# Optimization experiments

Hardware: AMD Instinct MI355X
Metric: run time of the kernel (lower is better)

Reference implementation:

```python
import jax, jax.numpy as jnp
import numpy as np

B = 4096
INPUT_DIM = 1024
ARG_IN = 8
IN_HIDDEN = 64
OUT_HIDDEN = [4096, 4096, 4096]
NUM_CELL_TYPES = 16
NUM_CLASSES = 10
LN_EPS = 1e-5


def _xavier(key, shape):
    # shape = (..., fan_in, fan_out); xavier uniform like torch init
    fan_in, fan_out = shape[-2], shape[-1]
    lim = float(np.sqrt(6.0 / (fan_in + fan_out)))
    return jax.random.uniform(key, shape, jnp.float32, -lim, lim)


def setup_inputs() -> dict:
    key = jax.random.key(0)
    ks = jax.random.split(key, 12)
    prev = OUT_HIDDEN[0] // ARG_IN  # 512
    inp = {
        "x": jax.random.normal(ks[0], (B, INPUT_DIM), jnp.float32),
        "labels": jax.random.randint(ks[1], (B,), 0, NUM_CLASSES),
        # outer nets (stored as (in, out))
        "Wout0": _xavier(ks[2], (INPUT_DIM, OUT_HIDDEN[0])),
        "bout0": jnp.zeros((OUT_HIDDEN[0],), jnp.float32),
        "Wout1": _xavier(ks[3], (prev, OUT_HIDDEN[1])),
        "bout1": jnp.zeros((OUT_HIDDEN[1],), jnp.float32),
        "Wout2": _xavier(ks[4], (prev, OUT_HIDDEN[2])),
        "bout2": jnp.zeros((OUT_HIDDEN[2],), jnp.float32),
        # per-cell-type inner MLPs, stacked over group dim T
        "W1": _xavier(ks[5], (NUM_CELL_TYPES, ARG_IN, IN_HIDDEN)),
        "b1": jnp.zeros((NUM_CELL_TYPES, IN_HIDDEN), jnp.float32),
        "W2": _xavier(ks[6], (NUM_CELL_TYPES, IN_HIDDEN, IN_HIDDEN)),
        "b2": jnp.zeros((NUM_CELL_TYPES, IN_HIDDEN), jnp.float32),
        "W3": _xavier(ks[7], (NUM_CELL_TYPES, IN_HIDDEN, 1))[..., 0],  # (T, H)
        "b3": jnp.zeros((NUM_CELL_TYPES,), jnp.float32),
        # output head
        "Wfc": _xavier(ks[8], (prev, NUM_CLASSES)),
        "bfc": jnp.zeros((NUM_CLASSES,), jnp.float32),
    }
    return inp


def _layernorm(x):
    mu = jnp.mean(x, axis=-1, keepdims=True)
    var = jnp.var(x, axis=-1, keepdims=True)
    return (x - mu) * jax.lax.rsqrt(var + LN_EPS)


def _inner_mlps(out, W1, b1, W2, b2, W3, b3):
    # out: (B, D) with D = T * Cg * ARG_IN; grouped tiny MLPs, vectorized over T
    bsz = out.shape[0]
    z = out.reshape(bsz, NUM_CELL_TYPES, -1, ARG_IN)  # (B, T, Cg, A)
    h = jax.nn.relu(jnp.einsum("btca,tah->btch", z, W1) + b1[None, :, None, :])
    h = jax.nn.relu(jnp.einsum("btch,thk->btck", h, W2) + b2[None, :, None, :])
    y = jnp.einsum("btch,th->btc", h, W3) + b3[None, :, None]  # (B, T, Cg)
    return y.reshape(bsz, -1)  # (B, T*Cg)


def reference(x, labels, Wout0, bout0, Wout1, bout1, Wout2, bout2,
              W1, b1, W2, b2, W3, b3, Wfc, bfc):
    outs = [(Wout0, bout0), (Wout1, bout1), (Wout2, bout2)]
    out = x.reshape(x.shape[0], -1)
    for W, b in outs:
        out = _layernorm(out @ W + b)
        out = _inner_mlps(out, W1, b1, W2, b2, W3, b3)
        # dropout p=0.0 -> identity
    logits = out @ Wfc + bfc  # (B, num_classes)
    logp = jax.nn.log_softmax(logits, axis=-1)
    loss = -jnp.mean(jnp.take_along_axis(logp, labels[:, None], axis=1))
    return logits, loss
```

## Files before the change

kernel.cpp:

```cpp
#include <hip/hip_runtime.h>
#include <hip/hip_bf16.h>
#include <math.h>

constexpr int BATCH   = 4096;
constexpr int NCLS    = 10;
constexpr int NHID    = 4096;
constexpr int PREV    = 512;
constexpr int NTYPES  = 16;
constexpr int CG      = 32;
constexpr float LN_EPS = 1e-5f;

typedef __attribute__((ext_vector_type(8))) short short8;
typedef __attribute__((ext_vector_type(4))) float f32x4;

__global__ __launch_bounds__(256)
void gemm_mfma_kernel(const __hip_bfloat16* __restrict__ A,
                      const __hip_bfloat16* __restrict__ BT,
                      const float* __restrict__ bias,
                      float* __restrict__ C,
                      int N, int K) {
  __shared__ __hip_bfloat16 As[128 * 32];
  __shared__ __hip_bfloat16 Bs[128 * 32];
  const int tid  = threadIdx.x;
  const int wid  = tid >> 6;
  const int lane = tid & 63;
  const int row0 = blockIdx.y * 128;
  const int col0 = blockIdx.x * 128;
  const int wrow = (wid >> 1) * 64;
  const int wcol = (wid & 1) * 64;

  f32x4 acc[4][4] = {};

  const int sr = wid * 32;
  const int lr = lane >> 2;
  const int lc = (lane & 3) * 8;

  const int fr = lane & 15;
  const int fo = (lane >> 4) * 8;

  for (int k0 = 0; k0 < K; k0 += 32) {
    const __hip_bfloat16* ga0 = A  + (size_t)(row0 + sr +      lr) * K + k0 + lc;
    const __hip_bfloat16* ga1 = A  + (size_t)(row0 + sr + 16 + lr) * K + k0 + lc;
    const __hip_bfloat16* gb0 = BT + (size_t)(col0 + sr +      lr) * K + k0 + lc;
    const __hip_bfloat16* gb1 = BT + (size_t)(col0 + sr + 16 + lr) * K + k0 + lc;
    __builtin_amdgcn_global_load_lds((const __attribute__((address_space(1))) void*)ga0,
                                     (__attribute__((address_space(3))) void*)&As[(sr     ) * 32], 16, 0, 0);
    __builtin_amdgcn_global_load_lds((const __attribute__((address_space(1))) void*)ga1,
                                     (__attribute__((address_space(3))) void*)&As[(sr + 16) * 32], 16, 0, 0);
    __builtin_amdgcn_global_load_lds((const __attribute__((address_space(1))) void*)gb0,
                                     (__attribute__((address_space(3))) void*)&Bs[(sr     ) * 32], 16, 0, 0);
    __builtin_amdgcn_global_load_lds((const __attribute__((address_space(1))) void*)gb1,
                                     (__attribute__((address_space(3))) void*)&Bs[(sr + 16) * 32], 16, 0, 0);
    __syncthreads();

    short8 af[4], bfr[4];
    #pragma unroll
    for (int i = 0; i < 4; ++i)
      af[i] = *reinterpret_cast<const short8*>(&As[(wrow + i * 16 + fr) * 32 + fo]);
    #pragma unroll
    for (int j = 0; j < 4; ++j)
      bfr[j] = *reinterpret_cast<const short8*>(&Bs[(wcol + j * 16 + fr) * 32 + fo]);

    #pragma unroll
    for (int i = 0; i < 4; ++i)
      #pragma unroll
      for (int j = 0; j < 4; ++j)
        acc[i][j] = __builtin_amdgcn_mfma_f32_16x16x32_bf16(af[i], bfr[j], acc[i][j], 0, 0, 0);
    __syncthreads();
  }

  #pragma unroll
  for (int j = 0; j < 4; ++j) {
    const int cc = col0 + wcol + j * 16 + (lane & 15);
    const float bv = bias[cc];
    #pragma unroll
    for (int i = 0; i < 4; ++i) {
      const int rr = row0 + wrow + i * 16 + (lane >> 4) * 4;
      #pragma unroll
      for (int r = 0; r < 4; ++r)
        C[(size_t)(rr + r) * N + cc] = acc[i][j][r] + bv;
    }
  }
}

__global__ __launch_bounds__(256)
void cvt_bf16_kernel(const float* __restrict__ in, __hip_bfloat16* __restrict__ out, int n) {
  const int i = (blockIdx.x * 256 + threadIdx.x) * 4;
  if (i >= n) return;
  const float4 v = *reinterpret_cast<const float4*>(&in[i]);
  __hip_bfloat16 t[4];
  t[0] = __float2bfloat16(v.x); t[1] = __float2bfloat16(v.y);
  t[2] = __float2bfloat16(v.z); t[3] = __float2bfloat16(v.w);
  *reinterpret_cast<ushort4*>(&out[i]) = *reinterpret_cast<const ushort4*>(t);
}

__global__ __launch_bounds__(256)
void transpose_cvt_kernel(const float* __restrict__ W, __hip_bfloat16* __restrict__ WT,
                          int K, int N) {
  __shared__ __hip_bfloat16 tile[64][65];
  const int tid = threadIdx.x;
  const int kt = blockIdx.y * 64, nt = blockIdx.x * 64;
  const int cn = tid & 63;
  for (int r = tid >> 6; r < 64; r += 4)
    tile[cn][r] = __float2bfloat16(W[(size_t)(kt + r) * N + nt + cn]);
  __syncthreads();
  for (int r = tid >> 6; r < 64; r += 4)
    WT[(size_t)(nt + r) * K + kt + cn] = tile[r][cn];
}

__global__ __launch_bounds__(256)
void prep_weights_kernel(const float* __restrict__ W2, const float* __restrict__ W1,
                         __hip_bfloat16* __restrict__ W2Tb,
                         __hip_bfloat16* __restrict__ W1b,
                         float* __restrict__ swsum) {
  const int t = blockIdx.x;
  for (int idx = threadIdx.x; idx < 64 * 64; idx += 256) {
    const int n = idx >> 6, h = idx & 63;
    W2Tb[t * 4096 + n * 64 + h] = __float2bfloat16(W2[t * 4096 + h * 64 + n]);
  }
  for (int idx = threadIdx.x; idx < 512; idx += 256) {
    const int n = idx >> 3, k = idx & 7;
    W1b[t * 512 + idx] = __float2bfloat16(W1[t * 512 + k * 64 + n]);
  }
  if (threadIdx.x < 64) {
    float s = 0.f;
    #pragma unroll
    for (int k = 0; k < 8; ++k) s += W1[t * 512 + k * 64 + threadIdx.x];
    swsum[t * 64 + threadIdx.x] = s;
  }
}

__global__ __launch_bounds__(256)
void ln_stats_kernel(const float* __restrict__ X, float2* __restrict__ stats) {
  const int lane = threadIdx.x & 63;
  const int row  = blockIdx.x * 4 + (threadIdx.x >> 6);
  const float* p = X + (size_t)row * NHID;
  float s = 0.f, ss = 0.f;
  #pragma unroll
  for (int i = 0; i < 16; ++i) {
    const float4 v = *reinterpret_cast<const float4*>(&p[i * 256 + lane * 4]);
    s  += v.x + v.y + v.z + v.w;
    ss += v.x * v.x + v.y * v.y + v.z * v.z + v.w * v.w;
  }
  #pragma unroll
  for (int off = 32; off; off >>= 1) { s += __shfl_xor(s, off); ss += __shfl_xor(ss, off); }
  if (lane == 0) {
    const float mu = s * (1.f / 4096.f);
    float2 st;
    st.x = mu;
    st.y = rsqrtf(ss * (1.f / 4096.f) - mu * mu + LN_EPS);
    stats[row] = st;
  }
}

__global__ __launch_bounds__(256, 2)
void inner_type_kernel(const float* __restrict__ X,
                       const float2* __restrict__ stats,
                       float* __restrict__ out,
                       __hip_bfloat16* __restrict__ outb,
                       const __hip_bfloat16* __restrict__ W2Tb,
                       const __hip_bfloat16* __restrict__ W1b,
                       const float* __restrict__ swsum,
                       const float* __restrict__ b1,
                       const float* __restrict__ b2,
                       const float* __restrict__ W3, const float* __restrict__ b3) {
  __shared__ __hip_bfloat16 H1s[128 * 64];
  const int tid  = threadIdx.x;
  const int lane = tid & 63;
  const int wvid = tid >> 6;
  const int t    = blockIdx.y;
  const int r0   = blockIdx.x * 64;

  const int fc  = lane & 15;
  const int fq  = lane >> 4;
  const bool ld = (fq == 0);

  const float* zcol = X + t * 256 + fc * 8;

#define LOAD_Z(zr, itv)                                                        \
  if (ld) {                                                                    \
    const float* zb_ = zcol + (size_t)(r0 + (itv) * 4 + wvid) * NHID;          \
    *reinterpret_cast<float4*>(&zr[0])  = *reinterpret_cast<const float4*>(zb_);          \
    *reinterpret_cast<float4*>(&zr[4])  = *reinterpret_cast<const float4*>(zb_ + 4);      \
    *reinterpret_cast<float4*>(&zr[8])  = *reinterpret_cast<const float4*>(zb_ + 128);    \
    *reinterpret_cast<float4*>(&zr[12]) = *reinterpret_cast<const float4*>(zb_ + 132);    \
  }

  float zA[16], zB[16];
  #pragma unroll
  for (int i = 0; i < 16; ++i) { zA[i] = 0.f; zB[i] = 0.f; }
  float2 stA, stB;
  LOAD_Z(zA, 0);
  stA = stats[r0 + wvid];

  short8 w1frag[4];
  #pragma unroll
  for (int nf = 0; nf < 4; ++nf) {
    short8 v = {};
    if (ld) v = *reinterpret_cast<const short8*>(&W1b[(size_t)t * 512 + (nf * 16 + fc) * 8]);
    w1frag[nf] = v;
  }

  short8 bfrag[4][2];
  #pragma unroll
  for (int cf = 0; cf < 4; ++cf)
    #pragma unroll
    for (int ks = 0; ks < 2; ++ks)
      bfrag[cf][ks] = *reinterpret_cast<const short8*>(
          &W2Tb[(size_t)t * 4096 + (cf * 16 + fc) * 64 + ks * 32 + fq * 8]);

  float4 b1q[4], swq[4];
  #pragma unroll
  for (int nf = 0; nf < 4; ++nf) {
    b1q[nf] = *reinterpret_cast<const float4*>(&b1[t * 64 + nf * 16 + fq * 4]);
    swq[nf] = *reinterpret_cast<const float4*>(&swsum[t * 64 + nf * 16 + fq * 4]);
  }

  float b2v[4], w3v[4];
  #pragma unroll
  for (int cf = 0; cf < 4; ++cf) {
    b2v[cf] = b2[t * 64 + cf * 16 + fc];
    w3v[cf] = W3[t * 64 + cf * 16 + fc];
  }
  const float yb = b3[t];

#define BODY(zr, stv, itv)                                                     \
  {                                                                            \
    const int row_ = r0 + (itv) * 4 + wvid;                                    \
    const float rs_ = stv.y;                                                   \
    const float c1_ = -stv.x * rs_;                                            \
            \
    short8 zf[2];                                                              \
    {                                                                          \
      union { short8 v; __hip_bfloat16 e[8]; } p0, p1;                         \
      _Pragma("unroll")                                                        \
      for (int q = 0; q < 8; ++q) {                                            \
        p0.e[q] = __float2bfloat16(zr[q]);                                     \
        p1.e[q] = __float2bfloat16(zr[8 + q]);                                 \
      }                                                                        \
      zf[0] = p0.v; zf[1] = p1.v;                                              \
    }                                                                          \
                  \
    f32x4 pC[4][2] = {};                                                       \
    _Pragma("unroll")                                                          \
    for (int nf = 0; nf < 4; ++nf) {                                           \
      pC[nf][0] = __builtin_amdgcn_mfma_f32_16x16x32_bf16(w1frag[nf], zf[0], pC[nf][0], 0, 0, 0); \
      pC[nf][1] = __builtin_amdgcn_mfma_f32_16x16x32_bf16(w1frag[nf], zf[1], pC[nf][1], 0, 0, 0); \
    }                                                                          \
        \
    _Pragma("unroll")                                                          \
    for (int nf = 0; nf < 4; ++nf) {                                           \
      const float bx = fmaf(c1_, swq[nf].x, b1q[nf].x);                        \
      const float by = fmaf(c1_, swq[nf].y, b1q[nf].y);                        \
      const float bz = fmaf(c1_, swq[nf].z, b1q[nf].z);                        \
      const float bw = fmaf(c1_, swq[nf].w, b1q[nf].w);                        \
      _Pragma("unroll")                                                        \
      for (int ci = 0; ci < 2; ++ci) {                                         \
        union { uint2 u; __hip_bfloat16 e[4]; } pk_;                           \
        pk_.e[0] = __float2bfloat16(fmaxf(fmaf(rs_, pC[nf][ci][0], bx), 0.f)); \
        pk_.e[1] = __float2bfloat16(fmaxf(fmaf(rs_, pC[nf][ci][1], by), 0.f)); \
        pk_.e[2] = __float2bfloat16(fmaxf(fmaf(rs_, pC[nf][ci][2], bz), 0.f)); \
        pk_.e[3] = __float2bfloat16(fmaxf(fmaf(rs_, pC[nf][ci][3], bw), 0.f)); \
        const int cell_ = wvid * 32 + ci * 16 + fc;                            \
        const int boff_ = cell_ * 128 + ((nf * 32 + fq * 8) ^ ((cell_ & 7) << 4)); \
        *reinterpret_cast<uint2*>((char*)H1s + boff_) = pk_.u;                 \
      }                                                                        \
    }                                                                          \
                  \
    f32x4 acc[2][4] = {};                                                      \
    _Pragma("unroll")                                                          \
    for (int ks = 0; ks < 2; ++ks) {                                           \
      short8 a0_, a1_;                                                         \
      {                                                                        \
        const int hrow_ = wvid * 32 + fc;                                      \
        a0_ = *reinterpret_cast<const short8*>(                                \
            &H1s[hrow_ * 64 + ((ks * 32 + fq * 8) ^ ((hrow_ & 7) << 3))]);     \
      }                                                                        \
      {                                                                        \
        const int hrow_ = wvid * 32 + 16 + fc;                                 \
        a1_ = *reinterpret_cast<const short8*>(                                \
            &H1s[hrow_ * 64 + ((ks * 32 + fq * 8) ^ ((hrow_ & 7) << 3))]);     \
      }                                                                        \
      _Pragma("unroll")                                                        \
      for (int cf = 0; cf < 4; ++cf) {                                         \
        acc[0][cf] = __builtin_amdgcn_mfma_f32_16x16x32_bf16(a0_, bfrag[cf][ks], acc[0][cf], 0, 0, 0); \
        acc[1][cf] = __builtin_amdgcn_mfma_f32_16x16x32_bf16(a1_, bfrag[cf][ks], acc[1][cf], 0, 0, 0); \
      }                                                                        \
    }                                                                          \
                                                              \
    float p[2][4];                                                             \
    _Pragma("unroll")                                                          \
    for (int rf = 0; rf < 2; ++rf)                                             \
      _Pragma("unroll")                                                        \
      for (int r = 0; r < 4; ++r) {                                            \
        float s_ = 0.f;                                                        \
        _Pragma("unroll")                                                      \
        for (int cf = 0; cf < 4; ++cf)                                         \
          s_ = fmaf(fmaxf(acc[rf][cf][r] + b2v[cf], 0.f), w3v[cf], s_);        \
        s_ += __shfl_xor(s_, 1);                                               \
        s_ += __shfl_xor(s_, 2);                                               \
        s_ += __shfl_xor(s_, 4);                                               \
        s_ += __shfl_xor(s_, 8);                                               \
        p[rf][r] = s_;                                                         \
      }                                                                        \
    if (fc == 0) {                                                             \
      _Pragma("unroll")                                                        \
      for (int rf = 0; rf < 2; ++rf)                                           \
        _Pragma("unroll")                                                      \
        for (int r = 0; r < 4; ++r) {                                          \
          const int c_ = rf * 16 + fq * 4 + r;                                 \
          const float y_ = p[rf][r] + yb;                                      \
          const size_t oidx_ = (size_t)row_ * PREV + t * CG + c_;              \
          if (out) out[oidx_] = y_;                                            \
          outb[oidx_] = __float2bfloat16(y_);                                  \
        }                                                                      \
    }                                                                          \
  }

  #pragma unroll 1
  for (int it2 = 0; it2 < 8; ++it2) {
    const int itA = it2 * 2;
    LOAD_Z(zB, itA + 1);
    stB = stats[r0 + (itA + 1) * 4 + wvid];
    BODY(zA, stA, itA);
    if (it2 < 7) {
      LOAD_Z(zA, itA + 2);
      stA = stats[r0 + (itA + 2) * 4 + wvid];
    }
    BODY(zB, stB, itA + 1);
  }
#undef LOAD_Z
#undef BODY
}

__global__ __launch_bounds__(64)
void head_kernel(const float* __restrict__ Y, const float* __restrict__ Wfc,
                 const float* __restrict__ bfc, const int* __restrict__ labels,
                 float* __restrict__ logits, float* __restrict__ rowloss) {
  const int b = blockIdx.x;
  const int lane = threadIdx.x;
  const float* yr = Y + (size_t)b * PREV;
  float acc[NCLS] = {};
  for (int k = lane; k < PREV; k += 64) {
    const float yv = yr[k];
    #pragma unroll
    for (int cI = 0; cI < NCLS; ++cI) acc[cI] = fmaf(yv, Wfc[k * NCLS + cI], acc[cI]);
  }
  #pragma unroll
  for (int cI = 0; cI < NCLS; ++cI) {
    #pragma unroll
    for (int off = 32; off; off >>= 1) acc[cI] += __shfl_down(acc[cI], off);
  }
  if (lane == 0) {
    float l[NCLS];
    float m = -1e30f;
    #pragma unroll
    for (int cI = 0; cI < NCLS; ++cI) { l[cI] = acc[cI] + bfc[cI]; m = fmaxf(m, l[cI]); }
    float se = 0.f;
    #pragma unroll
    for (int cI = 0; cI < NCLS; ++cI) se += __expf(l[cI] - m);
    const float lse = m + __logf(se);
    #pragma unroll
    for (int cI = 0; cI < NCLS; ++cI) logits[(size_t)b * NCLS + cI] = l[cI];
    const int lab = labels[b];
    float picked = 0.f;
    #pragma unroll
    for (int cI = 0; cI < NCLS; ++cI) picked += (cI == lab) ? l[cI] : 0.f;
    rowloss[b] = lse - picked;
  }
}

__global__ __launch_bounds__(256)
void loss_reduce_kernel(const float* __restrict__ rowloss, float* __restrict__ loss_out) {
  float s = 0.f;
  for (int i = threadIdx.x; i < BATCH; i += 256) s += rowloss[i];
  #pragma unroll
  for (int off = 32; off; off >>= 1) s += __shfl_down(s, off);
  __shared__ float sb[4];
  if ((threadIdx.x & 63) == 0) sb[threadIdx.x >> 6] = s;
  __syncthreads();
  if (threadIdx.x == 0) loss_out[0] = (sb[0] + sb[1] + sb[2] + sb[3]) * (1.f / BATCH);
}

extern "C" void kernel_launch(void* const* d_in, const int* in_sizes, int n_in,
                              void* d_out, int out_size, void* d_ws, size_t ws_size,
                              hipStream_t stream) {
  const float* x      = (const float*)d_in[0];
  const int*   labels = (const int*)  d_in[1];
  const float* Wout0  = (const float*)d_in[2];
  const float* bout0  = (const float*)d_in[3];
  const float* Wout1  = (const float*)d_in[4];
  const float* bout1  = (const float*)d_in[5];
  const float* Wout2  = (const float*)d_in[6];
  const float* bout2  = (const float*)d_in[7];
  const float* W1     = (const float*)d_in[8];
  const float* b1     = (const float*)d_in[9];
  const float* W2     = (const float*)d_in[10];
  const float* b2     = (const float*)d_in[11];
  const float* W3     = (const float*)d_in[12];
  const float* b3     = (const float*)d_in[13];
  const float* Wfc    = (const float*)d_in[14];
  const float* bfc    = (const float*)d_in[15];

  char* ws = (char*)d_ws;
  float*          Abuf    = (float*)(ws);
  float*          Ybuf    = (float*)(ws + ((size_t)64 << 20));
  __hip_bfloat16* Ybf     = (__hip_bfloat16*)(ws + ((size_t)72 << 20));
  __hip_bfloat16* xbf     = (__hip_bfloat16*)(ws + ((size_t)76 << 20));
  __hip_bfloat16* WT0     = (__hip_bfloat16*)(ws + ((size_t)84 << 20));
  __hip_bfloat16* WT1     = (__hip_bfloat16*)(ws + ((size_t)92 << 20));
  __hip_bfloat16* WT2     = (__hip_bfloat16*)(ws + ((size_t)96 << 20));
  __hip_bfloat16* W2Tb    = (__hip_bfloat16*)(ws + ((size_t)100 << 20));
  __hip_bfloat16* W1b     = (__hip_bfloat16*)(ws + ((size_t)100 << 20) + (128 << 10));
  float*          swsum   = (float*)(ws + ((size_t)100 << 20) + (192 << 10));
  float*          rowloss = (float*)(ws + ((size_t)101 << 20));
  float2*         stats   = (float2*)(ws + ((size_t)101 << 20) + (256 << 10));

  float* logits = (float*)d_out;
  float* loss   = logits + (size_t)BATCH * NCLS;

  cvt_bf16_kernel<<<dim3(BATCH * 1024 / 4 / 256), dim3(256), 0, stream>>>(x, xbf, BATCH * 1024);
  transpose_cvt_kernel<<<dim3(NHID / 64, 1024 / 64), dim3(256), 0, stream>>>(Wout0, WT0, 1024, NHID);
  transpose_cvt_kernel<<<dim3(NHID / 64, PREV / 64), dim3(256), 0, stream>>>(Wout1, WT1, PREV, NHID);
  transpose_cvt_kernel<<<dim3(NHID / 64, PREV / 64), dim3(256), 0, stream>>>(Wout2, WT2, PREV, NHID);
  prep_weights_kernel<<<dim3(NTYPES), dim3(256), 0, stream>>>(W2, W1, W2Tb, W1b, swsum);

  const dim3 ggrid(NHID / 128, BATCH / 128), gblk(256);
  const dim3 sgrid(BATCH / 4), sblk(256);
  const dim3 igrid(BATCH / 64, NTYPES), iblk(256);

  gemm_mfma_kernel<<<ggrid, gblk, 0, stream>>>(xbf, WT0, bout0, Abuf, NHID, 1024);
  ln_stats_kernel<<<sgrid, sblk, 0, stream>>>(Abuf, stats);
  inner_type_kernel<<<igrid, iblk, 0, stream>>>(Abuf, stats, nullptr, Ybf, W2Tb, W1b, swsum, b1, b2, W3, b3);
  gemm_mfma_kernel<<<ggrid, gblk, 0, stream>>>(Ybf, WT1, bout1, Abuf, NHID, PREV);
  ln_stats_kernel<<<sgrid, sblk, 0, stream>>>(Abuf, stats);
  inner_type_kernel<<<igrid, iblk, 0, stream>>>(Abuf, stats, nullptr, Ybf, W2Tb, W1b, swsum, b1, b2, W3, b3);
  gemm_mfma_kernel<<<ggrid, gblk, 0, stream>>>(Ybf, WT2, bout2, Abuf, NHID, PREV);
  ln_stats_kernel<<<sgrid, sblk, 0, stream>>>(Abuf, stats);
  inner_type_kernel<<<igrid, iblk, 0, stream>>>(Abuf, stats, Ybuf, Ybf, W2Tb, W1b, swsum, b1, b2, W3, b3);

  head_kernel<<<dim3(BATCH), dim3(64), 0, stream>>>(Ybuf, Wfc, bfc, labels, logits, rowloss);
  loss_reduce_kernel<<<dim3(1), dim3(256), 0, stream>>>(rowloss, loss);
}
```

Baseline: 380.4 us.

## Fuse LayerNorm statistics into GEMM epilogue and store activations as bf16

The GEMM epilogue now writes its output as bf16 instead of fp32 and computes per-row partial sums and sums of squares for each column block. A small reduce kernel turns those partials into mean and rstd, replacing the full-row stats pass that reread the fp32 matrix. The inner MLP kernel reads bf16 directly, which removes its in-register conversion, and it is relaunched with half the rows per block at higher occupancy. The intent is to cut HBM traffic for the large intermediate. The trade-off is that pre-LN values are rounded to bf16, and the variance uses single-pass sum and sum-of-squares accumulation.

```diff
diff --git a/kernel.cpp b/kernel.cpp
--- a/kernel.cpp
+++ b/kernel.cpp
@@ -8,19 +8,22 @@
 constexpr int PREV    = 512;
 constexpr int NTYPES  = 16;
 constexpr int CG      = 32;
+constexpr int NCB     = NHID / 128;
 constexpr float LN_EPS = 1e-5f;
 
 typedef __attribute__((ext_vector_type(8))) short short8;
 typedef __attribute__((ext_vector_type(4))) float f32x4;
 
 __global__ __launch_bounds__(256)
-void gemm_mfma_kernel(const __hip_bfloat16* __restrict__ A,
-                      const __hip_bfloat16* __restrict__ BT,
-                      const float* __restrict__ bias,
-                      float* __restrict__ C,
-                      int N, int K) {
+void gemm_ln_kernel(const __hip_bfloat16* __restrict__ A,
+                    const __hip_bfloat16* __restrict__ BT,
+                    const float* __restrict__ bias,
+                    __hip_bfloat16* __restrict__ Cb,
+                    float2* __restrict__ partials,
+                    int K) {
   __shared__ __hip_bfloat16 As[128 * 32];
   __shared__ __hip_bfloat16 Bs[128 * 32];
+  __shared__ float2 sbuf[2][128];
   const int tid  = threadIdx.x;
   const int wid  = tid >> 6;
   const int lane = tid & 63;
@@ -36,7 +39,8 @@
   const int lc = (lane & 3) * 8;
 
   const int fr = lane & 15;
-  const int fo = (lane >> 4) * 8;
+  const int lq = lane >> 4;
+  const int fo = lq * 8;
 
   for (int k0 = 0; k0 < K; k0 += 32) {
     const __hip_bfloat16* ga0 = A  + (size_t)(row0 + sr +      lr) * K + k0 + lc;
@@ -69,18 +73,53 @@
     __syncthreads();
   }
 
+  float sA[4][4] = {}, sQ[4][4] = {};
   #pragma unroll
   for (int j = 0; j < 4; ++j) {
-    const int cc = col0 + wcol + j * 16 + (lane & 15);
+    const int cc = col0 + wcol + j * 16 + fr;
     const float bv = bias[cc];
     #pragma unroll
     for (int i = 0; i < 4; ++i) {
-      const int rr = row0 + wrow + i * 16 + (lane >> 4) * 4;
+      const int rr = row0 + wrow + i * 16 + lq * 4;
       #pragma unroll
-      for (int r = 0; r < 4; ++r)
-        C[(size_t)(rr + r) * N + cc] = acc[i][j][r] + bv;
+      for (int r = 0; r < 4; ++r) {
+        const float v = acc[i][j][r] + bv;
+        Cb[(size_t)(rr + r) * NHID + cc] = __float2bfloat16(v);
+        sA[i][r] += v;
+        sQ[i][r] = fmaf(v, v, sQ[i][r]);
+      }
     }
   }
+  #pragma unroll
+  for (int i = 0; i < 4; ++i)
+    #pragma unroll
+    for (int r = 0; r < 4; ++r) {
+      float sv = sA[i][r], sq = sQ[i][r];
+      sv += __shfl_xor(sv, 1); sq += __shfl_xor(sq, 1);
+      sv += __shfl_xor(sv, 2); sq += __shfl_xor(sq, 2);
+      sv += __shfl_xor(sv, 4); sq += __shfl_xor(sq, 4);
+      sv += __shfl_xor(sv, 8); sq += __shfl_xor(sq, 8);
+      if (fr == 0) sbuf[wid & 1][wrow + i * 16 + lq * 4 + r] = make_float2(sv, sq);
+    }
+  __syncthreads();
+  for (int idx = tid; idx < 128; idx += 256) {
+    const float2 a = sbuf[0][idx], b = sbuf[1][idx];
+    partials[(size_t)(row0 + idx) * NCB + blockIdx.x] = make_float2(a.x + b.x, a.y + b.y);
+  }
+}
+
+__global__ __launch_bounds__(256)
+void stats_reduce_kernel(const float2* __restrict__ partials, float2* __restrict__ stats) {
+  const int row = blockIdx.x * 256 + threadIdx.x;
+  const float2* p = partials + (size_t)row * NCB;
+  float s = 0.f, ss = 0.f;
+  #pragma unroll
+  for (int cb = 0; cb < NCB; ++cb) { const float2 v = p[cb]; s += v.x; ss += v.y; }
+  const float mu = s * (1.f / 4096.f);
+  float2 st;
+  st.x = mu;
+  st.y = rsqrtf(ss * (1.f / 4096.f) - mu * mu + LN_EPS);
+  stats[row] = st;
 }
 
 __global__ __launch_bounds__(256)
@@ -130,31 +169,8 @@
   }
 }
 
-__global__ __launch_bounds__(256)
-void ln_stats_kernel(const float* __restrict__ X, float2* __restrict__ stats) {
-  const int lane = threadIdx.x & 63;
-  const int row  = blockIdx.x * 4 + (threadIdx.x >> 6);
-  const float* p = X + (size_t)row * NHID;
-  float s = 0.f, ss = 0.f;
-  #pragma unroll
-  for (int i = 0; i < 16; ++i) {
-    const float4 v = *reinterpret_cast<const float4*>(&p[i * 256 + lane * 4]);
-    s  += v.x + v.y + v.z + v.w;
-    ss += v.x * v.x + v.y * v.y + v.z * v.z + v.w * v.w;
-  }
-  #pragma unroll
-  for (int off = 32; off; off >>= 1) { s += __shfl_xor(s, off); ss += __shfl_xor(ss, off); }
-  if (lane == 0) {
-    const float mu = s * (1.f / 4096.f);
-    float2 st;
-    st.x = mu;
-    st.y = rsqrtf(ss * (1.f / 4096.f) - mu * mu + LN_EPS);
-    stats[row] = st;
-  }
-}
-
-__global__ __launch_bounds__(256, 2)
-void inner_type_kernel(const float* __restrict__ X,
+__global__ __launch_bounds__(256, 3)
+void inner_type_kernel(const __hip_bfloat16* __restrict__ Xb,
                        const float2* __restrict__ stats,
                        float* __restrict__ out,
                        __hip_bfloat16* __restrict__ outb,
@@ -169,28 +185,24 @@
   const int lane = tid & 63;
   const int wvid = tid >> 6;
   const int t    = blockIdx.y;
-  const int r0   = blockIdx.x * 64;
+  const int r0   = blockIdx.x * 32;
 
   const int fc  = lane & 15;
   const int fq  = lane >> 4;
   const bool ld = (fq == 0);
 
-  const float* zcol = X + t * 256 + fc * 8;
-
-#define LOAD_Z(zr, itv)                                                        \
+  const __hip_bfloat16* zcol = Xb + t * 256 + fc * 8;
+
+#define LOAD_Z(zf0, zf1, itv)                                                  \
   if (ld) {                                                                    \
-    const float* zb_ = zcol + (size_t)(r0 + (itv) * 4 + wvid) * NHID;          \
-    *reinterpret_cast<float4*>(&zr[0])  = *reinterpret_cast<const float4*>(zb_);          \
-    *reinterpret_cast<float4*>(&zr[4])  = *reinterpret_cast<const float4*>(zb_ + 4);      \
-    *reinterpret_cast<float4*>(&zr[8])  = *reinterpret_cast<const float4*>(zb_ + 128);    \
-    *reinterpret_cast<float4*>(&zr[12]) = *reinterpret_cast<const float4*>(zb_ + 132);    \
-  }
-
-  float zA[16], zB[16];
-  #pragma unroll
-  for (int i = 0; i < 16; ++i) { zA[i] = 0.f; zB[i] = 0.f; }
+    const __hip_bfloat16* zb_ = zcol + (size_t)(r0 + (itv) * 4 + wvid) * NHID; \
+    zf0 = *reinterpret_cast<const short8*>(zb_);                               \
+    zf1 = *reinterpret_cast<const short8*>(zb_ + 128);                         \
+  }
+
+  short8 zfA0 = {}, zfA1 = {}, zfB0 = {}, zfB1 = {};
   float2 stA, stB;
-  LOAD_Z(zA, 0);
+  LOAD_Z(zfA0, zfA1, 0);
   stA = stats[r0 + wvid];
 
   short8 w1frag[4];
@@ -224,30 +236,19 @@
   }
   const float yb = b3[t];
 
-#define BODY(zr, stv, itv)                                                     \
+#define BODY(zf0, zf1, stv, itv)                                               \
   {                                                                            \
     const int row_ = r0 + (itv) * 4 + wvid;                                    \
     const float rs_ = stv.y;                                                   \
     const float c1_ = -stv.x * rs_;                                            \
-            \
-    short8 zf[2];                                                              \
-    {                                                                          \
-      union { short8 v; __hip_bfloat16 e[8]; } p0, p1;                         \
-      _Pragma("unroll")                                                        \
-      for (int q = 0; q < 8; ++q) {                                            \
-        p0.e[q] = __float2bfloat16(zr[q]);                                     \
-        p1.e[q] = __float2bfloat16(zr[8 + q]);                                 \
-      }                                                                        \
-      zf[0] = p0.v; zf[1] = p1.v;                                              \
-    }                                                                          \
-                  \
+                   \
     f32x4 pC[4][2] = {};                                                       \
     _Pragma("unroll")                                                          \
     for (int nf = 0; nf < 4; ++nf) {                                           \
-      pC[nf][0] = __builtin_amdgcn_mfma_f32_16x16x32_bf16(w1frag[nf], zf[0], pC[nf][0], 0, 0, 0); \
-      pC[nf][1] = __builtin_amdgcn_mfma_f32_16x16x32_bf16(w1frag[nf], zf[1], pC[nf][1], 0, 0, 0); \
+      pC[nf][0] = __builtin_amdgcn_mfma_f32_16x16x32_bf16(w1frag[nf], zf0, pC[nf][0], 0, 0, 0); \
+      pC[nf][1] = __builtin_amdgcn_mfma_f32_16x16x32_bf16(w1frag[nf], zf1, pC[nf][1], 0, 0, 0); \
     }                                                                          \
-        \
+       \
     _Pragma("unroll")                                                          \
     for (int nf = 0; nf < 4; ++nf) {                                           \
       const float bx = fmaf(c1_, swq[nf].x, b1q[nf].x);                        \
@@ -266,7 +267,7 @@
         *reinterpret_cast<uint2*>((char*)H1s + boff_) = pk_.u;                 \
       }                                                                        \
     }                                                                          \
-                  \
+                                        \
     f32x4 acc[2][4] = {};                                                      \
     _Pragma("unroll")                                                          \
     for (int ks = 0; ks < 2; ++ks) {                                           \
@@ -318,16 +319,16 @@
   }
 
   #pragma unroll 1
-  for (int it2 = 0; it2 < 8; ++it2) {
+  for (int it2 = 0; it2 < 4; ++it2) {
     const int itA = it2 * 2;
-    LOAD_Z(zB, itA + 1);
+    LOAD_Z(zfB0, zfB1, itA + 1);
     stB = stats[r0 + (itA + 1) * 4 + wvid];
-    BODY(zA, stA, itA);
-    if (it2 < 7) {
-      LOAD_Z(zA, itA + 2);
+    BODY(zfA0, zfA1, stA, itA);
+    if (it2 < 3) {
+      LOAD_Z(zfA0, zfA1, itA + 2);
       stA = stats[r0 + (itA + 2) * 4 + wvid];
     }
-    BODY(zB, stB, itA + 1);
+    BODY(zfB0, zfB1, stB, itA + 1);
   }
 #undef LOAD_Z
 #undef BODY
@@ -403,18 +404,19 @@
   const float* bfc    = (const float*)d_in[15];
 
   char* ws = (char*)d_ws;
-  float*          Abuf    = (float*)(ws);
-  float*          Ybuf    = (float*)(ws + ((size_t)64 << 20));
-  __hip_bfloat16* Ybf     = (__hip_bfloat16*)(ws + ((size_t)72 << 20));
-  __hip_bfloat16* xbf     = (__hip_bfloat16*)(ws + ((size_t)76 << 20));
-  __hip_bfloat16* WT0     = (__hip_bfloat16*)(ws + ((size_t)84 << 20));
-  __hip_bfloat16* WT1     = (__hip_bfloat16*)(ws + ((size_t)92 << 20));
-  __hip_bfloat16* WT2     = (__hip_bfloat16*)(ws + ((size_t)96 << 20));
-  __hip_bfloat16* W2Tb    = (__hip_bfloat16*)(ws + ((size_t)100 << 20));
-  __hip_bfloat16* W1b     = (__hip_bfloat16*)(ws + ((size_t)100 << 20) + (128 << 10));
-  float*          swsum   = (float*)(ws + ((size_t)100 << 20) + (192 << 10));
-  float*          rowloss = (float*)(ws + ((size_t)101 << 20));
-  float2*         stats   = (float2*)(ws + ((size_t)101 << 20) + (256 << 10));
+  __hip_bfloat16* Abf     = (__hip_bfloat16*)(ws);
+  float*          Ybuf    = (float*)(ws + ((size_t)32 << 20));
+  __hip_bfloat16* Ybf     = (__hip_bfloat16*)(ws + ((size_t)40 << 20));
+  __hip_bfloat16* xbf     = (__hip_bfloat16*)(ws + ((size_t)44 << 20));
+  __hip_bfloat16* WT0     = (__hip_bfloat16*)(ws + ((size_t)52 << 20));
+  __hip_bfloat16* WT1     = (__hip_bfloat16*)(ws + ((size_t)60 << 20));
+  __hip_bfloat16* WT2     = (__hip_bfloat16*)(ws + ((size_t)64 << 20));
+  __hip_bfloat16* W2Tb    = (__hip_bfloat16*)(ws + ((size_t)68 << 20));
+  __hip_bfloat16* W1b     = (__hip_bfloat16*)(ws + ((size_t)68 << 20) + (128 << 10));
+  float*          swsum   = (float*)(ws + ((size_t)68 << 20) + (192 << 10));
+  float2*         partials= (float2*)(ws + ((size_t)69 << 20));
+  float2*         stats   = (float2*)(ws + ((size_t)70 << 20));
+  float*          rowloss = (float*)(ws + ((size_t)71 << 20));
 
   float* logits = (float*)d_out;
   float* loss   = logits + (size_t)BATCH * NCLS;
@@ -426,18 +428,18 @@
   prep_weights_kernel<<<dim3(NTYPES), dim3(256), 0, stream>>>(W2, W1, W2Tb, W1b, swsum);
 
   const dim3 ggrid(NHID / 128, BATCH / 128), gblk(256);
-  const dim3 sgrid(BATCH / 4), sblk(256);
-  const dim3 igrid(BATCH / 64, NTYPES), iblk(256);
-
-  gemm_mfma_kernel<<<ggrid, gblk, 0, stream>>>(xbf, WT0, bout0, Abuf, NHID, 1024);
-  ln_stats_kernel<<<sgrid, sblk, 0, stream>>>(Abuf, stats);
-  inner_type_kernel<<<igrid, iblk, 0, stream>>>(Abuf, stats, nullptr, Ybf, W2Tb, W1b, swsum, b1, b2, W3, b3);
-  gemm_mfma_kernel<<<ggrid, gblk, 0, stream>>>(Ybf, WT1, bout1, Abuf, NHID, PREV);
-  ln_stats_kernel<<<sgrid, sblk, 0, stream>>>(Abuf, stats);
-  inner_type_kernel<<<igrid, iblk, 0, stream>>>(Abuf, stats, nullptr, Ybf, W2Tb, W1b, swsum, b1, b2, W3, b3);
-  gemm_mfma_kernel<<<ggrid, gblk, 0, stream>>>(Ybf, WT2, bout2, Abuf, NHID, PREV);
-  ln_stats_kernel<<<sgrid, sblk, 0, stream>>>(Abuf, stats);
-  inner_type_kernel<<<igrid, iblk, 0, stream>>>(Abuf, stats, Ybuf, Ybf, W2Tb, W1b, swsum, b1, b2, W3, b3);
+  const dim3 rgrid(BATCH / 256), rblk(256);
+  const dim3 igrid(BATCH / 32, NTYPES), iblk(256);
+
+  gemm_ln_kernel<<<ggrid, gblk, 0, stream>>>(xbf, WT0, bout0, Abf, partials, 1024);
+  stats_reduce_kernel<<<rgrid, rblk, 0, stream>>>(partials, stats);
+  inner_type_kernel<<<igrid, iblk, 0, stream>>>(Abf, stats, nullptr, Ybf, W2Tb, W1b, swsum, b1, b2, W3, b3);
+  gemm_ln_kernel<<<ggrid, gblk, 0, stream>>>(Ybf, WT1, bout1, Abf, partials, PREV);
+  stats_reduce_kernel<<<rgrid, rblk, 0, stream>>>(partials, stats);
+  inner_type_kernel<<<igrid, iblk, 0, stream>>>(Abf, stats, nullptr, Ybf, W2Tb, W1b, swsum, b1, b2, W3, b3);
+  gemm_ln_kernel<<<ggrid, gblk, 0, stream>>>(Ybf, WT2, bout2, Abf, partials, PREV);
+  stats_reduce_kernel<<<rgrid, rblk, 0, stream>>>(partials, stats);
+  inner_type_kernel<<<igrid, iblk, 0, stream>>>(Abf, stats, Ybuf, Ybf, W2Tb, W1b, swsum, b1, b2, W3, b3);
 
   head_kernel<<<dim3(BATCH), dim3(64), 0, stream>>>(Ybuf, Wfc, bfc, labels, logits, rowloss);
   loss_reduce_kernel<<<dim3(1), dim3(256), 0, stream>>>(rowloss, loss);
```

Result: faster. 358.2 us (-5.9%).
